# Kernel optimization log

Measured on AMD Instinct MI355X. Metric: run time of the kernel, lower is better.

The kernel has to match this reference:

```python
import jax, jax.numpy as jnp
import numpy as np

B, D, N = 16, 512, 1024


def setup_inputs() -> dict:
    key = jax.random.key(0)
    k1, k2, k3, k4, k5 = jax.random.split(key, 5)
    return {
        "src_embedding": jax.random.normal(k1, (B, D, N), dtype=jnp.float32),
        "tgt_embedding": jax.random.normal(k2, (B, D, N), dtype=jnp.float32),
        "src": jax.random.normal(k3, (B, 3, N), dtype=jnp.float32),
        "tgt": jax.random.normal(k4, (B, 3, N), dtype=jnp.float32),
        "temperature": jax.random.uniform(k5, (B,), dtype=jnp.float32),
    }


def reference(src_embedding, tgt_embedding, src, tgt, temperature):
    b, d, n = src_embedding.shape
    # scores = softmax(temp * (src_emb^T tgt_emb) / sqrt(d_k), dim=2)
    logits = jnp.einsum("bdn,bdm->bnm", src_embedding, tgt_embedding) / np.sqrt(d).astype(np.float32)
    scores = jax.nn.softmax(temperature.reshape(b, 1, 1) * logits, axis=2)  # [B,N,N]
    # src_corr = tgt @ scores^T  -> soft correspondences [B,3,N]
    src_corr = jnp.einsum("bdm,bnm->bdn", tgt, scores)
    src_mean = src.mean(axis=2, keepdims=True)            # [B,3,1]
    corr_mean = src_corr.mean(axis=2, keepdims=True)      # [B,3,1]
    src_c = src - src_mean
    corr_c = src_corr - corr_mean
    H = jnp.einsum("bin,bjn->bij", src_c, corr_c)         # [B,3,3] covariance
    # Kabsch with reflection fix (batched 3x3 SVD)
    u, s, vh = jnp.linalg.svd(H)
    v = jnp.swapaxes(vh, -1, -2)
    ut = jnp.swapaxes(u, -1, -2)
    det = jax.lax.stop_gradient(jnp.linalg.det(v @ ut))   # +/-1, constant in torch (.item())
    d3 = jnp.stack([jnp.ones_like(det), jnp.ones_like(det), det], axis=-1)  # [B,3]
    R = (v * d3[:, None, :]) @ ut                          # v @ diag(1,1,det) @ u^T
    t = (-R @ src_mean) + corr_mean                        # [B,3,1]
    return R, t.reshape(b, 3)
```

## Files before the change

### kernel.cpp

```cpp
#include <hip/hip_runtime.h>
#include <math.h>

#define BATCH 16
#define DIM 512
#define NPTS 1024

typedef __attribute__((ext_vector_type(8))) short short8;
typedef __attribute__((ext_vector_type(4))) float f32x4;

__device__ __forceinline__ unsigned short f2bf(float x) {
    unsigned u = __float_as_uint(x);
    unsigned r = (u + 0x7FFFu + ((u >> 16) & 1u)) >> 16;
    return (unsigned short)r;
}

__device__ __forceinline__ void load_lds16(const void* g, void* l) {
    __builtin_amdgcn_global_load_lds(
        (const __attribute__((address_space(1))) void*)g,
        (__attribute__((address_space(3))) void*)l, 16, 0, 0);
}

__device__ void kabsch_from_H(double H[3][3], const double sm[3], const double cm[3],
                              float* out, int b) {
    double C[3][3];
    for (int i = 0; i < 3; ++i)
        for (int j = 0; j < 3; ++j) {
            double s = 0;
            for (int k = 0; k < 3; ++k) s += H[k][i] * H[k][j];
            C[i][j] = s;
        }
    double V[3][3] = {{1, 0, 0}, {0, 1, 0}, {0, 0, 1}};
    for (int sweep = 0; sweep < 30; ++sweep) {
        const double offd = fabs(C[0][1]) + fabs(C[0][2]) + fabs(C[1][2]);
        const double diag = fabs(C[0][0]) + fabs(C[1][1]) + fabs(C[2][2]);
        if (offd <= 1e-15 * (diag + 1e-300)) break;
        for (int pq = 0; pq < 3; ++pq) {
            const int p = (pq == 2) ? 1 : 0;
            const int q = (pq == 0) ? 1 : 2;
            const double apq = C[p][q];
            if (fabs(apq) < 1e-300) continue;
            const double theta = (C[q][q] - C[p][p]) / (2.0 * apq);
            const double t_ = copysign(1.0, theta) / (fabs(theta) + sqrt(1.0 + theta * theta));
            const double c_ = 1.0 / sqrt(1.0 + t_ * t_);
            const double s_ = t_ * c_;
            const int r = 3 - p - q;
            const double cpp = C[p][p], cqq = C[q][q];
            C[p][p] = cpp - t_ * apq;
            C[q][q] = cqq + t_ * apq;
            C[p][q] = C[q][p] = 0.0;
            const double crp = C[r][p], crq = C[r][q];
            C[r][p] = C[p][r] = c_ * crp - s_ * crq;
            C[r][q] = C[q][r] = s_ * crp + c_ * crq;
            for (int k = 0; k < 3; ++k) {
                const double vkp = V[k][p], vkq = V[k][q];
                V[k][p] = c_ * vkp - s_ * vkq;
                V[k][q] = s_ * vkp + c_ * vkq;
            }
        }
    }
    double lam[3] = {C[0][0], C[1][1], C[2][2]};
    int i0 = 0, i1 = 1, i2 = 2, tswp;
    if (lam[i0] < lam[i1]) { tswp = i0; i0 = i1; i1 = tswp; }
    if (lam[i0] < lam[i2]) { tswp = i0; i0 = i2; i2 = tswp; }
    if (lam[i1] < lam[i2]) { tswp = i1; i1 = i2; i2 = tswp; }

    const double v0[3] = {V[0][i0], V[1][i0], V[2][i0]};
    const double v1[3] = {V[0][i1], V[1][i1], V[2][i1]};
    const double v2[3] = {V[0][i2], V[1][i2], V[2][i2]};
    const double detV = v0[0] * (v1[1] * v2[2] - v1[2] * v2[1])
                      - v0[1] * (v1[0] * v2[2] - v1[2] * v2[0])
                      + v0[2] * (v1[0] * v2[1] - v1[1] * v2[0]);

    double u0[3], u1[3], u2[3];
    for (int i = 0; i < 3; ++i)
        u0[i] = H[i][0] * v0[0] + H[i][1] * v0[1] + H[i][2] * v0[2];
    double n0 = sqrt(u0[0] * u0[0] + u0[1] * u0[1] + u0[2] * u0[2]);
    n0 = fmax(n0, 1e-300);
    u0[0] /= n0; u0[1] /= n0; u0[2] /= n0;
    for (int i = 0; i < 3; ++i)
        u1[i] = H[i][0] * v1[0] + H[i][1] * v1[1] + H[i][2] * v1[2];
    const double d01 = u0[0] * u1[0] + u0[1] * u1[1] + u0[2] * u1[2];
    u1[0] -= d01 * u0[0]; u1[1] -= d01 * u0[1]; u1[2] -= d01 * u0[2];
    double n1 = sqrt(u1[0] * u1[0] + u1[1] * u1[1] + u1[2] * u1[2]);
    n1 = fmax(n1, 1e-300);
    u1[0] /= n1; u1[1] /= n1; u1[2] /= n1;
    u2[0] = u0[1] * u1[2] - u0[2] * u1[1];
    u2[1] = u0[2] * u1[0] - u0[0] * u1[2];
    u2[2] = u0[0] * u1[1] - u0[1] * u1[0];

    double R[3][3];
    for (int a = 0; a < 3; ++a)
        for (int c = 0; c < 3; ++c)
            R[a][c] = v0[a] * u0[c] + v1[a] * u1[c] + detV * v2[a] * u2[c];

    for (int a = 0; a < 3; ++a) {
        const double tv = cm[a] - (R[a][0] * sm[0] + R[a][1] * sm[1] + R[a][2] * sm[2]);
        out[b * 9 + a * 3 + 0] = (float)R[a][0];
        out[b * 9 + a * 3 + 1] = (float)R[a][1];
        out[b * 9 + a * 3 + 2] = (float)R[a][2];
        out[BATCH * 9 + b * 3 + a] = (float)tv;
    }
}

__global__ __launch_bounds__(256) void transpose_bf16_kernel(
    const float* __restrict__ src_emb, const float* __restrict__ tgt_emb,
    unsigned short* __restrict__ AT, unsigned short* __restrict__ BT)
{
    const int bid = blockIdx.x;
    const int b  = bid >> 7;
    const int dt = (bid >> 4) & 7;
    const int nt = bid & 15;
    const int tid = threadIdx.x;

    __shared__ float tile[64][65];

    for (int pass = 0; pass < 2; ++pass) {
        const float* src = pass ? tgt_emb : src_emb;
        unsigned short* dst = pass ? BT : AT;

        const int lr = tid >> 4;
        const int c4 = (tid & 15) * 4;
#pragma unroll
        for (int q = 0; q < 4; ++q) {
            const int dl = lr + q * 16;
            const float4 v = *(const float4*)(src + ((size_t)(b * DIM + dt * 64 + dl)) * NPTS + nt * 64 + c4);
            tile[dl][c4 + 0] = v.x;
            tile[dl][c4 + 1] = v.y;
            tile[dl][c4 + 2] = v.z;
            tile[dl][c4 + 3] = v.w;
        }
        __syncthreads();

#pragma unroll
        for (int s = 0; s < 2; ++s) {
            const int nl = s * 32 + (tid >> 3);
            const int d8 = (tid & 7) * 8;
            union { unsigned short us[8]; uint4 q4; } pk;
#pragma unroll
            for (int k = 0; k < 8; ++k) pk.us[k] = f2bf(tile[d8 + k][nl]);
            *(uint4*)(dst + ((size_t)(b * NPTS + nt * 64 + nl)) * DIM + dt * 64 + d8) = pk.q4;
        }
        __syncthreads();
    }
}

#define AB_BYTES (64 * 64)
#define BB_BYTES (256 * 64)

__global__ __launch_bounds__(256, 4) void attn_corr_kernel(
    const unsigned short* __restrict__ AT, const unsigned short* __restrict__ BT,
    const float* __restrict__ tgt, const float* __restrict__ temperature,
    float* __restrict__ P)
{
    __shared__ char lds[2 * AB_BYTES + 2 * BB_BYTES];

    const int bid = blockIdx.x;
    const int b  = bid >> 6;
    const int inner = bid & 63;
    const int qt = inner >> 2;
    const int ms = inner & 3;
    const int tid = threadIdx.x;
    const int lane = tid & 63;
    const int wv = tid >> 6;

    const unsigned short* Abase = AT + ((size_t)b * NPTS + qt * 64) * DIM;
    const unsigned short* Bbase = BT + ((size_t)b * NPTS + ms * 256) * DIM;

    const int a_r  = wv * 16 + (lane >> 2);
    const int a_s  = lane & 3;
    const int a_cl = a_s ^ ((a_r >> 1) & 3);
    const size_t a_src_off = (size_t)a_r * DIM + a_cl * 8;

    int b_r[4], b_cl[4];
#pragma unroll
    for (int q = 0; q < 4; ++q) {
        b_r[q]  = q * 64 + wv * 16 + (lane >> 2);
        b_cl[q] = (lane & 3) ^ ((b_r[q] >> 1) & 3);
    }

    const int fp = lane & 15;
    const int fg = lane >> 4;

    f32x4 acc[4][4];
#pragma unroll
    for (int kt = 0; kt < 4; ++kt)
#pragma unroll
        for (int qj = 0; qj < 4; ++qj) acc[kt][qj] = (f32x4){0.f, 0.f, 0.f, 0.f};

    char* Ab0 = lds;
    char* Ab1 = lds + AB_BYTES;
    char* Bb0 = lds + 2 * AB_BYTES;
    char* Bb1 = lds + 2 * AB_BYTES + BB_BYTES;

#define STAGE(CH, ABUF, BBUF)                                                        \
    {                                                                                \
        const int d0_ = (CH) * 32;                                                   \
        load_lds16(Abase + a_src_off + d0_, (ABUF) + wv * 1024);                     \
        _Pragma("unroll")                                                            \
        for (int q = 0; q < 4; ++q)                                                  \
            load_lds16(Bbase + (size_t)b_r[q] * DIM + d0_ + b_cl[q] * 8,             \
                       (BBUF) + q * 4096 + wv * 1024);                               \
    }

#define COMPUTE(ABUF, BBUF)                                                          \
    {                                                                                \
        short8 kf[4], qf[4];                                                         \
        _Pragma("unroll")                                                            \
        for (int kt = 0; kt < 4; ++kt) {                                             \
            const int r = wv * 64 + kt * 16 + fp;                                    \
            const int cl = fg ^ ((r >> 1) & 3);                                      \
            kf[kt] = *(const short8*)((BBUF) + r * 64 + cl * 16);                    \
        }                                                                            \
        _Pragma("unroll")                                                            \
        for (int qj = 0; qj < 4; ++qj) {                                             \
            const int r = qj * 16 + fp;                                              \
            const int cl = fg ^ ((r >> 1) & 3);                                      \
            qf[qj] = *(const short8*)((ABUF) + r * 64 + cl * 16);                    \
        }                                                                            \
        _Pragma("unroll")                                                            \
        for (int kt = 0; kt < 4; ++kt)                                               \
            _Pragma("unroll")                                                        \
            for (int qj = 0; qj < 4; ++qj)                                           \
                acc[kt][qj] = __builtin_amdgcn_mfma_f32_16x16x32_bf16(               \
                    kf[kt], qf[qj], acc[kt][qj], 0, 0, 0);                           \
    }

    STAGE(0, Ab0, Bb0);
    __syncthreads();
#pragma unroll 2
    for (int ch = 0; ch < 16; ++ch) {
        if (ch & 1) {
            if (ch < 15) STAGE(ch + 1, Ab0, Bb0);
            COMPUTE(Ab1, Bb1);
        } else {
            if (ch < 15) STAGE(ch + 1, Ab1, Bb1);
            COMPUTE(Ab0, Bb0);
        }
        __syncthreads();
    }

    const float s2 = temperature[b] * (0.04419417382415922f * 1.4426950408889634f);
    const float* tb = tgt + (size_t)b * 3 * NPTS;

    float l[4]  = {0.f, 0.f, 0.f, 0.f};
    float a0[4] = {0.f, 0.f, 0.f, 0.f};
    float a1[4] = {0.f, 0.f, 0.f, 0.f};
    float a2[4] = {0.f, 0.f, 0.f, 0.f};

#pragma unroll
    for (int kt = 0; kt < 4; ++kt) {
        float t0[4], t1[4], t2[4];
#pragma unroll
        for (int reg = 0; reg < 4; ++reg) {
            const int m = ms * 256 + wv * 64 + kt * 16 + fg * 4 + reg;
            t0[reg] = tb[m];
            t1[reg] = tb[NPTS + m];
            t2[reg] = tb[2 * NPTS + m];
        }
#pragma unroll
        for (int qj = 0; qj < 4; ++qj) {
#pragma unroll
            for (int reg = 0; reg < 4; ++reg) {
                const float w = exp2f(acc[kt][qj][reg] * s2);
                l[qj]  += w;
                a0[qj] = fmaf(w, t0[reg], a0[qj]);
                a1[qj] = fmaf(w, t1[reg], a1[qj]);
                a2[qj] = fmaf(w, t2[reg], a2[qj]);
            }
        }
    }

    float* Pb = P + ((size_t)b * 16 + (ms * 4 + wv)) * 4 * NPTS;
#pragma unroll
    for (int qj = 0; qj < 4; ++qj) {
        float lv = l[qj], v0 = a0[qj], v1 = a1[qj], v2 = a2[qj];
        lv += __shfl_xor(lv, 16); lv += __shfl_xor(lv, 32);
        v0 += __shfl_xor(v0, 16); v0 += __shfl_xor(v0, 32);
        v1 += __shfl_xor(v1, 16); v1 += __shfl_xor(v1, 32);
        v2 += __shfl_xor(v2, 16); v2 += __shfl_xor(v2, 32);
        if (fg == 0) {
            const int n = qt * 64 + qj * 16 + fp;
            Pb[0 * NPTS + n] = lv;
            Pb[1 * NPTS + n] = v0;
            Pb[2 * NPTS + n] = v1;
            Pb[3 * NPTS + n] = v2;
        }
    }
}

__global__ __launch_bounds__(256) void merge_reduce_svd_kernel(
    const float* __restrict__ P, const float* __restrict__ src,
    float* __restrict__ out)
{
    const int b = blockIdx.x;
    const int tid = threadIdx.x;

    __shared__ float wred[4][9];
    __shared__ float meansh[6];

    float corr[4][3], sv[4][3];
    float cs0 = 0, cs1 = 0, cs2 = 0, ss0 = 0, ss1 = 0, ss2 = 0;

#pragma unroll
    for (int j = 0; j < 4; ++j) {
        const int n = tid + j * 256;
        float l = 0, a0 = 0, a1 = 0, a2 = 0;
        for (int pp = 0; pp < 16; ++pp) {
            const float* Pb = P + ((size_t)b * 16 + pp) * 4 * NPTS;
            l  += Pb[n];
            a0 += Pb[NPTS + n];
            a1 += Pb[2 * NPTS + n];
            a2 += Pb[3 * NPTS + n];
        }
        const float inv = 1.0f / l;
        corr[j][0] = a0 * inv; corr[j][1] = a1 * inv; corr[j][2] = a2 * inv;
        cs0 += corr[j][0]; cs1 += corr[j][1]; cs2 += corr[j][2];
        sv[j][0] = src[((size_t)b * 3 + 0) * NPTS + n];
        sv[j][1] = src[((size_t)b * 3 + 1) * NPTS + n];
        sv[j][2] = src[((size_t)b * 3 + 2) * NPTS + n];
        ss0 += sv[j][0]; ss1 += sv[j][1]; ss2 += sv[j][2];
    }

#pragma unroll
    for (int off = 1; off < 64; off <<= 1) {
        ss0 += __shfl_xor(ss0, off); ss1 += __shfl_xor(ss1, off); ss2 += __shfl_xor(ss2, off);
        cs0 += __shfl_xor(cs0, off); cs1 += __shfl_xor(cs1, off); cs2 += __shfl_xor(cs2, off);
    }
    const int wave = tid >> 6;
    if ((tid & 63) == 0) {
        wred[wave][0] = ss0; wred[wave][1] = ss1; wred[wave][2] = ss2;
        wred[wave][3] = cs0; wred[wave][4] = cs1; wred[wave][5] = cs2;
    }
    __syncthreads();
    if (tid < 6)
        meansh[tid] = (wred[0][tid] + wred[1][tid] + wred[2][tid] + wred[3][tid]) * (1.0f / NPTS);
    __syncthreads();
    const float sm0 = meansh[0], sm1 = meansh[1], sm2 = meansh[2];
    const float cm0 = meansh[3], cm1 = meansh[4], cm2 = meansh[5];

    float h[9] = {0, 0, 0, 0, 0, 0, 0, 0, 0};
#pragma unroll
    for (int j = 0; j < 4; ++j) {
        const float a0 = sv[j][0] - sm0, a1 = sv[j][1] - sm1, a2 = sv[j][2] - sm2;
        const float b0 = corr[j][0] - cm0, b1 = corr[j][1] - cm1, b2 = corr[j][2] - cm2;
        h[0] += a0 * b0; h[1] += a0 * b1; h[2] += a0 * b2;
        h[3] += a1 * b0; h[4] += a1 * b1; h[5] += a1 * b2;
        h[6] += a2 * b0; h[7] += a2 * b1; h[8] += a2 * b2;
    }
#pragma unroll
    for (int off = 1; off < 64; off <<= 1) {
#pragma unroll
        for (int j = 0; j < 9; ++j) h[j] += __shfl_xor(h[j], off);
    }
    __syncthreads();
    if ((tid & 63) == 0) {
#pragma unroll
        for (int j = 0; j < 9; ++j) wred[wave][j] = h[j];
    }
    __syncthreads();

    if (tid == 0) {
        double H[3][3];
        for (int i = 0; i < 3; ++i)
            for (int j = 0; j < 3; ++j)
                H[i][j] = (double)wred[0][i * 3 + j] + wred[1][i * 3 + j]
                        + wred[2][i * 3 + j] + wred[3][i * 3 + j];
        const double sm[3] = {sm0, sm1, sm2};
        const double cm[3] = {cm0, cm1, cm2};
        kabsch_from_H(H, sm, cm, out, b);
    }
}

__global__ __launch_bounds__(256) void flash_corr_kernel(
    const float* __restrict__ src_emb,
    const float* __restrict__ tgt_emb,
    const float* __restrict__ tgt,
    const float* __restrict__ temperature,
    float* __restrict__ corr)
{
    const int bid = blockIdx.x;
    const int b   = bid & 15;
    const int qt  = bid >> 4;
    const int n0  = qt * 64;
    const int tid = threadIdx.x;
    const int tx  = tid & 15;
    const int ty  = tid >> 4;

    const float scale = temperature[b] * (1.0f / sqrtf((float)DIM));

    __shared__ float As[2][32][64];
    __shared__ float Bs[2][32][64];
    __shared__ float Ts[3][64];

    const float* Abase  = src_emb + (size_t)b * DIM * NPTS + n0;
    const float* Bbatch = tgt_emb + (size_t)b * DIM * NPTS;
    const float* Tbatch = tgt     + (size_t)b * 3 * NPTS;

    const int dr0 = tid >> 4;
    const int dr1 = dr0 + 16;
    const int c4  = (tid & 15) * 4;

    float mrun[4], lpart[4], acc0[4], acc1[4], acc2[4];
#pragma unroll
    for (int r = 0; r < 4; ++r) {
        mrun[r] = -1e30f; lpart[r] = 0.0f;
        acc0[r] = 0.0f; acc1[r] = 0.0f; acc2[r] = 0.0f;
    }

    for (int mt = 0; mt < 16; ++mt) {
        const int m0 = mt * 64;
        const float* Bbase = Bbatch + m0;
        __syncthreads();
        if (tid < 192) {
            const int i = tid >> 6, mc = tid & 63;
            Ts[i][mc] = Tbatch[i * NPTS + m0 + mc];
        }
        {
            float4 a0 = *(const float4*)(Abase + (size_t)dr0 * NPTS + c4);
            float4 a1 = *(const float4*)(Abase + (size_t)dr1 * NPTS + c4);
            float4 b0 = *(const float4*)(Bbase + (size_t)dr0 * NPTS + c4);
            float4 b1 = *(const float4*)(Bbase + (size_t)dr1 * NPTS + c4);
            *(float4*)&As[0][dr0][c4] = a0;
            *(float4*)&As[0][dr1][c4] = a1;
            *(float4*)&Bs[0][dr0][c4] = b0;
            *(float4*)&Bs[0][dr1][c4] = b1;
        }
        __syncthreads();

        float S[4][4];
#pragma unroll
        for (int r = 0; r < 4; ++r)
#pragma unroll
            for (int c = 0; c < 4; ++c) S[r][c] = 0.0f;

        for (int ch = 0; ch < 16; ++ch) {
            const int buf = ch & 1;
            float4 a0n, a1n, b0n, b1n;
            if (ch < 15) {
                const float* Ab = Abase + (size_t)(ch + 1) * 32 * NPTS;
                const float* Bb = Bbase + (size_t)(ch + 1) * 32 * NPTS;
                a0n = *(const float4*)(Ab + (size_t)dr0 * NPTS + c4);
                a1n = *(const float4*)(Ab + (size_t)dr1 * NPTS + c4);
                b0n = *(const float4*)(Bb + (size_t)dr0 * NPTS + c4);
                b1n = *(const float4*)(Bb + (size_t)dr1 * NPTS + c4);
            }
#pragma unroll
            for (int dk = 0; dk < 32; ++dk) {
                const float4 av = *(const float4*)(&As[buf][dk][ty * 4]);
                const float4 bv = *(const float4*)(&Bs[buf][dk][tx * 4]);
                S[0][0] = fmaf(av.x, bv.x, S[0][0]);
                S[0][1] = fmaf(av.x, bv.y, S[0][1]);
                S[0][2] = fmaf(av.x, bv.z, S[0][2]);
                S[0][3] = fmaf(av.x, bv.w, S[0][3]);
                S[1][0] = fmaf(av.y, bv.x, S[1][0]);
                S[1][1] = fmaf(av.y, bv.y, S[1][1]);
                S[1][2] = fmaf(av.y, bv.z, S[1][2]);
                S[1][3] = fmaf(av.y, bv.w, S[1][3]);
                S[2][0] = fmaf(av.z, bv.x, S[2][0]);
                S[2][1] = fmaf(av.z, bv.y, S[2][1]);
                S[2][2] = fmaf(av.z, bv.z, S[2][2]);
                S[2][3] = fmaf(av.z, bv.w, S[2][3]);
                S[3][0] = fmaf(av.w, bv.x, S[3][0]);
                S[3][1] = fmaf(av.w, bv.y, S[3][1]);
                S[3][2] = fmaf(av.w, bv.z, S[3][2]);
                S[3][3] = fmaf(av.w, bv.w, S[3][3]);
            }
            __syncthreads();
            if (ch < 15) {
                *(float4*)&As[buf ^ 1][dr0][c4] = a0n;
                *(float4*)&As[buf ^ 1][dr1][c4] = a1n;
                *(float4*)&Bs[buf ^ 1][dr0][c4] = b0n;
                *(float4*)&Bs[buf ^ 1][dr1][c4] = b1n;
                __syncthreads();
            }
        }

#pragma unroll
        for (int r = 0; r < 4; ++r) {
            float z0 = S[r][0] * scale, z1 = S[r][1] * scale;
            float z2 = S[r][2] * scale, z3 = S[r][3] * scale;
            float mt_ = fmaxf(fmaxf(z0, z1), fmaxf(z2, z3));
#pragma unroll
            for (int off = 1; off < 16; off <<= 1)
                mt_ = fmaxf(mt_, __shfl_xor(mt_, off));
            const float mnew = fmaxf(mrun[r], mt_);
            const float f = expf(mrun[r] - mnew);
            lpart[r] *= f; acc0[r] *= f; acc1[r] *= f; acc2[r] *= f;
            const float w0 = expf(z0 - mnew);
            const float w1 = expf(z1 - mnew);
            const float w2 = expf(z2 - mnew);
            const float w3 = expf(z3 - mnew);
            lpart[r] += w0 + w1 + w2 + w3;
            const int mc = tx * 4;
            acc0[r] += w0 * Ts[0][mc] + w1 * Ts[0][mc+1] + w2 * Ts[0][mc+2] + w3 * Ts[0][mc+3];
            acc1[r] += w0 * Ts[1][mc] + w1 * Ts[1][mc+1] + w2 * Ts[1][mc+2] + w3 * Ts[1][mc+3];
            acc2[r] += w0 * Ts[2][mc] + w1 * Ts[2][mc+1] + w2 * Ts[2][mc+2] + w3 * Ts[2][mc+3];
            mrun[r] = mnew;
        }
    }

#pragma unroll
    for (int r = 0; r < 4; ++r) {
        float l = lpart[r], a0 = acc0[r], a1 = acc1[r], a2 = acc2[r];
#pragma unroll
        for (int off = 1; off < 16; off <<= 1) {
            l  += __shfl_xor(l,  off);
            a0 += __shfl_xor(a0, off);
            a1 += __shfl_xor(a1, off);
            a2 += __shfl_xor(a2, off);
        }
        if (tx == 0) {
            const int n = n0 + ty * 4 + r;
            const float inv = 1.0f / l;
            corr[((size_t)b * 3 + 0) * NPTS + n] = a0 * inv;
            corr[((size_t)b * 3 + 1) * NPTS + n] = a1 * inv;
            corr[((size_t)b * 3 + 2) * NPTS + n] = a2 * inv;
        }
    }
}

__global__ __launch_bounds__(256) void reduce_svd_kernel(
    const float* __restrict__ src,
    const float* __restrict__ corr,
    float* __restrict__ out)
{
    const int b = blockIdx.x;
    const int tid = threadIdx.x;

    __shared__ float wred[4][9];
    __shared__ float meansh[6];

    const float* sp = src  + (size_t)b * 3 * NPTS;
    const float* cp = corr + (size_t)b * 3 * NPTS;

    float ss0 = 0, ss1 = 0, ss2 = 0, cs0 = 0, cs1 = 0, cs2 = 0;
    for (int n = tid; n < NPTS; n += 256) {
        ss0 += sp[n]; ss1 += sp[NPTS + n]; ss2 += sp[2 * NPTS + n];
        cs0 += cp[n]; cs1 += cp[NPTS + n]; cs2 += cp[2 * NPTS + n];
    }
#pragma unroll
    for (int off = 1; off < 64; off <<= 1) {
        ss0 += __shfl_xor(ss0, off); ss1 += __shfl_xor(ss1, off); ss2 += __shfl_xor(ss2, off);
        cs0 += __shfl_xor(cs0, off); cs1 += __shfl_xor(cs1, off); cs2 += __shfl_xor(cs2, off);
    }
    const int wave = tid >> 6;
    if ((tid & 63) == 0) {
        wred[wave][0] = ss0; wred[wave][1] = ss1; wred[wave][2] = ss2;
        wred[wave][3] = cs0; wred[wave][4] = cs1; wred[wave][5] = cs2;
    }
    __syncthreads();
    if (tid < 6)
        meansh[tid] = (wred[0][tid] + wred[1][tid] + wred[2][tid] + wred[3][tid]) * (1.0f / NPTS);
    __syncthreads();
    const float sm0 = meansh[0], sm1 = meansh[1], sm2 = meansh[2];
    const float cm0 = meansh[3], cm1 = meansh[4], cm2 = meansh[5];

    float h[9] = {0, 0, 0, 0, 0, 0, 0, 0, 0};
    for (int n = tid; n < NPTS; n += 256) {
        const float a0 = sp[n] - sm0, a1 = sp[NPTS + n] - sm1, a2 = sp[2 * NPTS + n] - sm2;
        const float b0 = cp[n] - cm0, b1 = cp[NPTS + n] - cm1, b2 = cp[2 * NPTS + n] - cm2;
        h[0] += a0 * b0; h[1] += a0 * b1; h[2] += a0 * b2;
        h[3] += a1 * b0; h[4] += a1 * b1; h[5] += a1 * b2;
        h[6] += a2 * b0; h[7] += a2 * b1; h[8] += a2 * b2;
    }
#pragma unroll
    for (int off = 1; off < 64; off <<= 1) {
#pragma unroll
        for (int j = 0; j < 9; ++j) h[j] += __shfl_xor(h[j], off);
    }
    __syncthreads();
    if ((tid & 63) == 0) {
#pragma unroll
        for (int j = 0; j < 9; ++j) wred[wave][j] = h[j];
    }
    __syncthreads();

    if (tid == 0) {
        double H[3][3];
        for (int i = 0; i < 3; ++i)
            for (int j = 0; j < 3; ++j)
                H[i][j] = (double)wred[0][i * 3 + j] + wred[1][i * 3 + j]
                        + wred[2][i * 3 + j] + wred[3][i * 3 + j];
        const double sm[3] = {sm0, sm1, sm2};
        const double cm[3] = {cm0, cm1, cm2};
        kabsch_from_H(H, sm, cm, out, b);
    }
}

extern "C" void kernel_launch(void* const* d_in, const int* in_sizes, int n_in,
                              void* d_out, int out_size, void* d_ws, size_t ws_size,
                              hipStream_t stream) {
    const float* src_emb = (const float*)d_in[0];
    const float* tgt_emb = (const float*)d_in[1];
    const float* src     = (const float*)d_in[2];
    const float* tgt     = (const float*)d_in[3];
    const float* temp    = (const float*)d_in[4];
    float* out = (float*)d_out;

    const size_t AT_BYTES = (size_t)BATCH * NPTS * DIM * 2;
    const size_t P_BYTES  = (size_t)BATCH * 16 * 4 * NPTS * 4;

    if (ws_size >= 2 * AT_BYTES + P_BYTES) {
        unsigned short* AT = (unsigned short*)d_ws;
        unsigned short* BT = (unsigned short*)((char*)d_ws + AT_BYTES);
        float* P = (float*)((char*)d_ws + 2 * AT_BYTES);

        transpose_bf16_kernel<<<dim3(BATCH * 8 * 16), dim3(256), 0, stream>>>(
            src_emb, tgt_emb, AT, BT);
        attn_corr_kernel<<<dim3(BATCH * 16 * 4), dim3(256), 0, stream>>>(
            AT, BT, tgt, temp, P);
        merge_reduce_svd_kernel<<<dim3(BATCH), dim3(256), 0, stream>>>(P, src, out);
    } else {
        float* corr = (float*)d_ws;
        flash_corr_kernel<<<dim3(BATCH * (NPTS / 64)), dim3(256), 0, stream>>>(
            src_emb, tgt_emb, tgt, temp, corr);
        reduce_svd_kernel<<<dim3(BATCH), dim3(256), 0, stream>>>(src, corr, out);
    }
}
```

Before: 64.95 us.

## Deepen LDS pipeline to four stages with explicit vmcnt waits and MFMA priority

Replaces the double-buffered LDS staging with a four-buffer ring that keeps three chunks of loads in flight. Fine-grained s_waitcnt vmcnt counts replace the full __syncthreads, and s_setprio raises wave priority around the MFMA block. The extra LDS cuts launch bounds from four to two blocks per CU, trading occupancy for latency hiding. The hand-counted vmcnt values rely on exactly five loads per stage, so any change in load count would silently break the synchronisation.

Result: faster. 61.09 us (-6.0%).

```diff
diff --git a/kernel.cpp b/kernel.cpp
--- a/kernel.cpp
+++ b/kernel.cpp
@@ -144,15 +144,15 @@
     }
 }
 
-#define AB_BYTES (64 * 64)
-#define BB_BYTES (256 * 64)
-
-__global__ __launch_bounds__(256, 4) void attn_corr_kernel(
+#define AB_BYTES 4096
+#define BB_BYTES 16384
+
+__global__ __launch_bounds__(256, 2) void attn_corr_kernel(
     const unsigned short* __restrict__ AT, const unsigned short* __restrict__ BT,
     const float* __restrict__ tgt, const float* __restrict__ temperature,
     float* __restrict__ P)
 {
-    __shared__ char lds[2 * AB_BYTES + 2 * BB_BYTES];
+    __shared__ char lds[4 * (AB_BYTES + BB_BYTES)];
 
     const int bid = blockIdx.x;
     const int b  = bid >> 6;
@@ -167,8 +167,7 @@
     const unsigned short* Bbase = BT + ((size_t)b * NPTS + ms * 256) * DIM;
 
     const int a_r  = wv * 16 + (lane >> 2);
-    const int a_s  = lane & 3;
-    const int a_cl = a_s ^ ((a_r >> 1) & 3);
+    const int a_cl = (lane & 3) ^ ((a_r >> 1) & 3);
     const size_t a_src_off = (size_t)a_r * DIM + a_cl * 8;
 
     int b_r[4], b_cl[4];
@@ -187,10 +186,11 @@
 #pragma unroll
         for (int qj = 0; qj < 4; ++qj) acc[kt][qj] = (f32x4){0.f, 0.f, 0.f, 0.f};
 
-    char* Ab0 = lds;
-    char* Ab1 = lds + AB_BYTES;
-    char* Bb0 = lds + 2 * AB_BYTES;
-    char* Bb1 = lds + 2 * AB_BYTES + BB_BYTES;
+    char* AbP[4] = {lds, lds + AB_BYTES, lds + 2 * AB_BYTES, lds + 3 * AB_BYTES};
+    char* BbP[4] = {lds + 4 * AB_BYTES,
+                    lds + 4 * AB_BYTES + BB_BYTES,
+                    lds + 4 * AB_BYTES + 2 * BB_BYTES,
+                    lds + 4 * AB_BYTES + 3 * BB_BYTES};
 
 #define STAGE(CH, ABUF, BBUF)                                                        \
     {                                                                                \
@@ -217,26 +217,30 @@
             const int cl = fg ^ ((r >> 1) & 3);                                      \
             qf[qj] = *(const short8*)((ABUF) + r * 64 + cl * 16);                    \
         }                                                                            \
+        __builtin_amdgcn_s_setprio(1);                                               \
         _Pragma("unroll")                                                            \
         for (int kt = 0; kt < 4; ++kt)                                               \
             _Pragma("unroll")                                                        \
             for (int qj = 0; qj < 4; ++qj)                                           \
                 acc[kt][qj] = __builtin_amdgcn_mfma_f32_16x16x32_bf16(               \
                     kf[kt], qf[qj], acc[kt][qj], 0, 0, 0);                           \
-    }
-
-    STAGE(0, Ab0, Bb0);
-    __syncthreads();
-#pragma unroll 2
+        __builtin_amdgcn_s_setprio(0);                                               \
+    }
+
+    STAGE(0, AbP[0], BbP[0]);
+    STAGE(1, AbP[1], BbP[1]);
+    STAGE(2, AbP[2], BbP[2]);
+
+#pragma unroll
     for (int ch = 0; ch < 16; ++ch) {
-        if (ch & 1) {
-            if (ch < 15) STAGE(ch + 1, Ab0, Bb0);
-            COMPUTE(Ab1, Bb1);
-        } else {
-            if (ch < 15) STAGE(ch + 1, Ab1, Bb1);
-            COMPUTE(Ab0, Bb0);
-        }
-        __syncthreads();
+        if (ch <= 13)      { asm volatile("s_waitcnt vmcnt(10)" ::: "memory"); }
+        else if (ch == 14) { asm volatile("s_waitcnt vmcnt(5)"  ::: "memory"); }
+        else               { asm volatile("s_waitcnt vmcnt(0)"  ::: "memory"); }
+        __builtin_amdgcn_s_barrier();
+        __builtin_amdgcn_sched_barrier(0);
+        if (ch + 3 < 16) STAGE(ch + 3, AbP[(ch + 3) & 3], BbP[(ch + 3) & 3]);
+        COMPUTE(AbP[ch & 3], BbP[ch & 3]);
+        __builtin_amdgcn_sched_barrier(0);
     }
 
     const float s2 = temperature[b] * (0.04419417382415922f * 1.4426950408889634f);
```
